# Performance work log

Measured on AMD Instinct MI355X. Metric: run time of the kernel, lower is better.

## Reference

```python
import jax, jax.numpy as jnp
import numpy as np

T, D, H, Z = 16384, 100, 50, 64
LN_EPS = 1e-6


def _ln(x, s, b):
    m = x.mean(-1, keepdims=True)
    v = ((x - m) ** 2).mean(-1, keepdims=True)
    return (x - m) / jnp.sqrt(v + LN_EPS) * s + b


def _gru_ln_scan(y, Wi, Wh, ls, lb):
    # Precompute all input projections once: [T, 3H]
    xi = y @ Wi
    h0 = jnp.zeros((Wh.shape[0],), y.dtype)

    def step(h, xi_t):
        hh = h @ Wh
        xr, xz, xn = jnp.split(xi_t, 3)
        hr, hz, hn = jnp.split(hh, 3)
        r = jax.nn.sigmoid(_ln(xr, ls[0], lb[0]) + _ln(hr, ls[1], lb[1]))
        z = jax.nn.sigmoid(_ln(xz, ls[2], lb[2]) + _ln(hz, ls[3], lb[3]))
        n = jnp.tanh(_ln(xn, ls[4], lb[4]) + r * _ln(hn, ls[5], lb[5]))
        h_new = (1.0 - z) * n + z * h
        return h_new, h_new

    _, hs = jax.lax.scan(step, h0, xi)
    return hs  # [T, H]


def setup_inputs() -> dict:
    key = jax.random.key(0)
    ks = jax.random.split(key, 6)
    sI = 1.0 / jnp.sqrt(jnp.float32(D))
    sH = 1.0 / jnp.sqrt(jnp.float32(H))
    sD = 1.0 / jnp.sqrt(jnp.float32(2 * H))
    return {
        "y": jax.random.normal(ks[0], (T, D), jnp.float32),
        "Wi_f": jax.random.normal(ks[1], (D, 3 * H), jnp.float32) * sI,
        "Wh_f": jax.random.normal(ks[2], (H, 3 * H), jnp.float32) * sH,
        "ln_s_f": jnp.ones((6, H), jnp.float32),
        "ln_b_f": jnp.zeros((6, H), jnp.float32),
        "Wi_b": jax.random.normal(ks[3], (D, 3 * H), jnp.float32) * sI,
        "Wh_b": jax.random.normal(ks[4], (H, 3 * H), jnp.float32) * sH,
        "ln_s_b": jnp.ones((6, H), jnp.float32),
        "ln_b_b": jnp.zeros((6, H), jnp.float32),
        "Wd": jax.random.normal(ks[5], (2 * H, 2 * Z), jnp.float32) * sD,
        "bd": jnp.zeros((2 * Z,), jnp.float32),
    }


def reference(y, Wi_f, Wh_f, ln_s_f, ln_b_f, Wi_b, Wh_b, ln_s_b, ln_b_b, Wd, bd):
    fwd = _gru_ln_scan(y, Wi_f, Wh_f, ln_s_f, ln_b_f)                       # [T, H]
    bwd = jnp.flip(_gru_ln_scan(jnp.flip(y, 0), Wi_b, Wh_b, ln_s_b, ln_b_b), 0)
    cc = jnp.concatenate([fwd, bwd], axis=-1)                               # [T, 2H]
    out = cc @ Wd + bd                                                      # [T, 2Z]
    z = Wd.shape[1] // 2
    mu, vflat = out[:, :z], out[:, z:]
    ev = jnp.exp(vflat)
    eye = jnp.eye(z, dtype=y.dtype)
    Sigma = eye * (ev + 1e-6)[:, None, :]   # diag(exp(v)+1e-6) per timestep
    J = eye * (1.0 / ev)[:, None, :]        # diag(1/exp(v)) per timestep
    h = mu / ev                             # J @ mu for diagonal J
    return Sigma, mu, J, h
```

## Files before the change

### kernel.cpp

```cpp
#include <hip/hip_runtime.h>

#define TT 16384
#define DD 100
#define HH 50
#define XG_STRIDE 160

#define CL 16
#define NCHUNK (TT / CL)
#define BURN 64

#define XROWS 16
#define NFILLB 512

#define WS_XG 0

#define OFF_MU ((size_t)TT * 64 * 64)
#define OFF_J  (OFF_MU + (size_t)TT * 64)
#define OFF_H  (OFF_J + (size_t)TT * 64 * 64)

typedef float v2f __attribute__((ext_vector_type(2)));
typedef float v4f __attribute__((ext_vector_type(4)));

template <int CTRL>
__device__ __forceinline__ float dpp_add(float x) {
    const int y = __builtin_amdgcn_update_dpp(
        0, __builtin_bit_cast(int, x), CTRL, 0xf, 0xf, false);
    return x + __builtin_bit_cast(float, y);
}
__device__ __forceinline__ float wave_sum63(float x) {
    x = dpp_add<0x111>(x);
    x = dpp_add<0x112>(x);
    x = dpp_add<0x114>(x);
    x = dpp_add<0x118>(x);
    x = dpp_add<0x142>(x);
    x = dpp_add<0x143>(x);
    return x;
}
__device__ __forceinline__ float bcast_lane(float x, int l) {
    return __builtin_bit_cast(float,
        __builtin_amdgcn_readlane(__builtin_bit_cast(int, x), l));
}
__device__ __forceinline__ float fold_mean(float w, int L, int lane) {
    const float s = wave_sum63(w);
    const float cm = bcast_lane(s, 63) * 0.02f;
    return (lane == L) ? cm : w;
}

__global__ __launch_bounds__(192) void xprep_kernel(
    const float* __restrict__ y,
    const float* __restrict__ Wi_f, const float* __restrict__ Wi_b,
    const float* __restrict__ ls_f, const float* __restrict__ lb_f,
    const float* __restrict__ ls_b, const float* __restrict__ lb_b,
    float* __restrict__ xg, float* __restrict__ out)
{
    const int tid = threadIdx.x;
    const int dir = blockIdx.y;

    if (dir == 2) {
        const int fb = blockIdx.x;
        v4f* __restrict__ base = (fb < NFILLB)
            ? (v4f*)out : (v4f*)(out + OFF_J);
        const int sub = fb & (NFILLB - 1);
        const long QS = (long)TT * 1024;
        const v4f zz = {0.f, 0.f, 0.f, 0.f};
        const long stride = (long)NFILLB * 192;
        for (long q = (long)sub * 192 + tid; q < QS; q += stride)
            __builtin_nontemporal_store(zz, &base[q]);
        return;
    }

    const int t0  = blockIdx.x * XROWS;
    const float* __restrict__ Wi = dir ? Wi_b : Wi_f;
    const float* __restrict__ ls = dir ? ls_b : ls_f;
    const float* __restrict__ lb = dir ? lb_b : lb_f;

    __shared__ __align__(16) float yst[DD][XROWS];

    for (int idx = tid; idx < DD * XROWS; idx += 192) {
        const int r = idx / DD;
        const int k = idx - r * DD;
        const int row = dir ? (TT - 1 - (t0 + r)) : (t0 + r);
        yst[k][r] = y[(size_t)row * DD + k];
    }
    __syncthreads();

    const int g    = tid >> 6;
    const int lane = tid & 63;
    const bool act = lane < HH;
    const int col  = g * 50 + (act ? lane : 0);

    float acc[XROWS];
    #pragma unroll
    for (int r = 0; r < XROWS; ++r) acc[r] = 0.f;

    #pragma unroll 2
    for (int k = 0; k < DD; ++k) {
        const float w = Wi[k * 150 + col];
        const float4* yr = (const float4*)&yst[k][0];
        const float4 A = yr[0], B = yr[1], C = yr[2], D = yr[3];
        acc[0]  = fmaf(w, A.x, acc[0]);  acc[1]  = fmaf(w, A.y, acc[1]);
        acc[2]  = fmaf(w, A.z, acc[2]);  acc[3]  = fmaf(w, A.w, acc[3]);
        acc[4]  = fmaf(w, B.x, acc[4]);  acc[5]  = fmaf(w, B.y, acc[5]);
        acc[6]  = fmaf(w, B.z, acc[6]);  acc[7]  = fmaf(w, B.w, acc[7]);
        acc[8]  = fmaf(w, C.x, acc[8]);  acc[9]  = fmaf(w, C.y, acc[9]);
        acc[10] = fmaf(w, C.z, acc[10]); acc[11] = fmaf(w, C.w, acc[11]);
        acc[12] = fmaf(w, D.x, acc[12]); acc[13] = fmaf(w, D.y, acc[13]);
        acc[14] = fmaf(w, D.z, acc[14]); acc[15] = fmaf(w, D.w, acc[15]);
    }

    const int lrow = g * 100 + (act ? lane : 0);
    const float sc = ls[lrow], bi = lb[lrow];
    #pragma unroll
    for (int r = 0; r < XROWS; ++r) {
        const float a  = act ? acc[r] : 0.f;
        const float s  = bcast_lane(wave_sum63(a), 63);
        const float s2 = bcast_lane(wave_sum63(a * a), 63);
        const float mean = s * 0.02f;
        const float var  = s2 * 0.02f - mean * mean;
        const float rstd = rsqrtf(var + 1e-6f);
        if (act)
            xg[((size_t)dir * TT + (t0 + r)) * XG_STRIDE + col] =
                (acc[r] - mean) * rstd * sc + bi;
    }
}

__global__ __launch_bounds__(128, 1) void scanhead_kernel(
    const float* __restrict__ xg,
    const float* __restrict__ Wh_f, const float* __restrict__ Wh_b,
    const float* __restrict__ ls_f, const float* __restrict__ lb_f,
    const float* __restrict__ ls_b, const float* __restrict__ lb_b,
    const float* __restrict__ Wd, const float* __restrict__ bd,
    float* __restrict__ out)
{
    const int tid  = threadIdx.x;
    const int wid  = tid >> 6;
    const int lane = tid & 63;
    const int dir  = wid;
    const int blk  = blockIdx.x;

    const float* __restrict__ Wh = dir ? Wh_b : Wh_f;
    const float* __restrict__ ls = dir ? ls_b : ls_f;
    const float* __restrict__ lb = dir ? lb_b : lb_f;
    const float* __restrict__ xgd = xg + (size_t)dir * TT * XG_STRIDE;

    const bool act = lane < HH;

    const int cstart = dir ? (TT - (blk + 1) * CL) : (blk * CL);
    const int rbase  = blk * CL;
    const int t0 = (cstart >= BURN) ? (cstart - BURN) : 0;
    const int tend = cstart + CL;

    __shared__ __align__(16) float ccs[DD][CL];
    __shared__ __align__(16) float os[CL][128];
    __shared__ __align__(16) float hb[2][52];
    if (lane < 52) hb[wid][lane] = 0.f;

    v2f wr2[26], wz2[26], wn2[26];
    #pragma unroll
    for (int p = 0; p < 26; ++p) {
        wr2[p] = (v2f){0.f, 0.f};
        wz2[p] = (v2f){0.f, 0.f};
        wn2[p] = (v2f){0.f, 0.f};
    }
    float s1 = 0.f, b1 = 0.f, s3 = 0.f, b3 = 0.f, s5 = 0.f, b5 = 0.f;
    if (act) {
        #pragma unroll
        for (int k = 0; k < HH; ++k) {
            const float a = Wh[k * 150 + lane];
            const float b = Wh[k * 150 + 50 + lane];
            const float c = Wh[k * 150 + 100 + lane];
            if (k & 1) { wr2[k >> 1].y = a; wz2[k >> 1].y = b; wn2[k >> 1].y = c; }
            else       { wr2[k >> 1].x = a; wz2[k >> 1].x = b; wn2[k >> 1].x = c; }
        }
        s1 = ls[50 + lane];  b1 = lb[50 + lane];
        s3 = ls[150 + lane]; b3 = lb[150 + lane];
        s5 = ls[250 + lane]; b5 = lb[250 + lane];
    }
    #pragma unroll
    for (int p = 0; p < 26; ++p) {
        wr2[p].x = fold_mean(wr2[p].x, 50, lane);
        wr2[p].y = fold_mean(wr2[p].y, 50, lane);
        wz2[p].x = fold_mean(wz2[p].x, 51, lane);
        wz2[p].y = fold_mean(wz2[p].y, 51, lane);
        wn2[p].x = fold_mean(wn2[p].x, 52, lane);
        wn2[p].y = fold_mean(wn2[p].y, 52, lane);
    }

    float hreg = 0.f;
    const int xl = act ? lane : 0;
    const float* __restrict__ x0 = xgd + (size_t)t0 * XG_STRIDE;
    float xr = x0[xl], xz = x0[50 + xl], xn = x0[100 + xl];
    float pxr = x0[XG_STRIDE + xl];
    float pxz = x0[XG_STRIDE + 50 + xl];
    float pxn = x0[XG_STRIDE + 100 + xl];

    #pragma unroll 1
    for (int t = t0; t < tend; ++t) {
        const int tp = (t + 2 < TT) ? (t + 2) : (TT - 1);
        const float* __restrict__ xp = xgd + (size_t)tp * XG_STRIDE;
        const float qxr = xp[xl], qxz = xp[50 + xl], qxn = xp[100 + xl];

        v2f ar0 = {0.f, 0.f}, ar1 = {0.f, 0.f};
        v2f az0 = {0.f, 0.f}, az1 = {0.f, 0.f};
        v2f an0 = {0.f, 0.f}, an1 = {0.f, 0.f};
        const float4* hb4 = reinterpret_cast<const float4*>(&hb[wid][0]);
        #pragma unroll
        for (int q = 0; q < 13; ++q) {
            const float4 hv = hb4[q];
            const v2f h0 = {hv.x, hv.y};
            const v2f h1 = {hv.z, hv.w};
            ar0 = __builtin_elementwise_fma(h0, wr2[2 * q],     ar0);
            ar1 = __builtin_elementwise_fma(h1, wr2[2 * q + 1], ar1);
            az0 = __builtin_elementwise_fma(h0, wz2[2 * q],     az0);
            az1 = __builtin_elementwise_fma(h1, wz2[2 * q + 1], az1);
            an0 = __builtin_elementwise_fma(h0, wn2[2 * q],     an0);
            an1 = __builtin_elementwise_fma(h1, wn2[2 * q + 1], an1);
        }
        const float ar = (ar0.x + ar0.y) + (ar1.x + ar1.y);
        const float az = (az0.x + az0.y) + (az1.x + az1.y);
        const float an = (an0.x + an0.y) + (an1.x + an1.y);

        const float mr = bcast_lane(ar, 50);
        const float mz = bcast_lane(az, 51);
        const float mn = bcast_lane(an, 52);

        const float qrv = act ? ar * ar : 0.f;
        const float qzv = act ? az * az : 0.f;
        const float qnv = act ? an * an : 0.f;
        const float Sr = bcast_lane(wave_sum63(qrv), 63);
        const float Sz = bcast_lane(wave_sum63(qzv), 63);
        const float Sn = bcast_lane(wave_sum63(qnv), 63);

        const float i50 = 0.02f;
        const float vr = fmaf(-mr, mr, Sr * i50);
        const float vz = fmaf(-mz, mz, Sz * i50);
        const float vn = fmaf(-mn, mn, Sn * i50);
        const float rr = rsqrtf(vr + 1e-6f);
        const float rz = rsqrtf(vz + 1e-6f);
        const float rn = rsqrtf(vn + 1e-6f);
        const float hrl = (ar - mr) * rr * s1 + b1;
        const float hzl = (az - mz) * rz * s3 + b3;
        const float hnl = (an - mn) * rn * s5 + b5;

        const float r = __builtin_amdgcn_rcpf(1.f + __expf(-(xr + hrl)));
        const float z = __builtin_amdgcn_rcpf(1.f + __expf(-(xz + hzl)));
        const float e2 = __expf(2.f * (xn + r * hnl));
        const float n = 1.f - 2.f * __builtin_amdgcn_rcpf(e2 + 1.f);
        const float hnew = fmaf(z, hreg - n, n);

        if (act) {
            hb[wid][lane] = hnew;
            if (t >= cstart) {
                const int rr2 = dir ? (TT - 1 - t - rbase) : (t - rbase);
                ccs[dir * 50 + lane][rr2] = hnew;
            }
        }
        hreg = act ? hnew : 0.f;

        xr = pxr; xz = pxz; xn = pxn;
        pxr = qxr; pxz = qxz; pxn = qxn;
    }

    __syncthreads();

    const int j = tid;
    float acc[CL];
    const float bj = bd[j];
    #pragma unroll
    for (int r = 0; r < CL; ++r) acc[r] = bj;

    #pragma unroll 2
    for (int k = 0; k < DD; ++k) {
        const float w = Wd[k * 128 + j];
        const float4* cr = (const float4*)&ccs[k][0];
        const float4 A = cr[0], B4 = cr[1], C4 = cr[2], D4 = cr[3];
        acc[0]  = fmaf(w, A.x,  acc[0]);  acc[1]  = fmaf(w, A.y,  acc[1]);
        acc[2]  = fmaf(w, A.z,  acc[2]);  acc[3]  = fmaf(w, A.w,  acc[3]);
        acc[4]  = fmaf(w, B4.x, acc[4]);  acc[5]  = fmaf(w, B4.y, acc[5]);
        acc[6]  = fmaf(w, B4.z, acc[6]);  acc[7]  = fmaf(w, B4.w, acc[7]);
        acc[8]  = fmaf(w, C4.x, acc[8]);  acc[9]  = fmaf(w, C4.y, acc[9]);
        acc[10] = fmaf(w, C4.z, acc[10]); acc[11] = fmaf(w, C4.w, acc[11]);
        acc[12] = fmaf(w, D4.x, acc[12]); acc[13] = fmaf(w, D4.y, acc[13]);
        acc[14] = fmaf(w, D4.z, acc[14]); acc[15] = fmaf(w, D4.w, acc[15]);
    }
    #pragma unroll
    for (int r = 0; r < CL; ++r) os[r][j] = acc[r];
    __syncthreads();

    if (j < 64) {
        const int d = j & 3;
        #pragma unroll
        for (int r = 0; r < CL; ++r) {
            const int t = rbase + r;
            const float mu  = os[r][j];
            const float evv = __expf(os[r][64 + j]);
            out[OFF_MU + (size_t)t * 64 + j] = mu;
            out[OFF_H  + (size_t)t * 64 + j] = mu / evv;
            const float se = evv + 1e-6f;
            float4 s4;
            s4.x = (d == 0) ? se : 0.f;  s4.y = (d == 1) ? se : 0.f;
            s4.z = (d == 2) ? se : 0.f;  s4.w = (d == 3) ? se : 0.f;
            ((float4*)out)[(size_t)t * 1024 + j * 16 + (j >> 2)] = s4;
        }
    } else {
        const int i = j - 64;
        const int d = i & 3;
        float4* __restrict__ jo4 = (float4*)(out + OFF_J);
        #pragma unroll
        for (int r = 0; r < CL; ++r) {
            const int t = rbase + r;
            const float evv = __expf(os[r][j]);
            const float je = 1.f / evv;
            float4 j4;
            j4.x = (d == 0) ? je : 0.f;  j4.y = (d == 1) ? je : 0.f;
            j4.z = (d == 2) ? je : 0.f;  j4.w = (d == 3) ? je : 0.f;
            jo4[(size_t)t * 1024 + i * 16 + (i >> 2)] = j4;
        }
    }
}

extern "C" void kernel_launch(void* const* d_in, const int* in_sizes, int n_in,
                              void* d_out, int out_size, void* d_ws, size_t ws_size,
                              hipStream_t stream)
{
    const float* y    = (const float*)d_in[0];
    const float* Wi_f = (const float*)d_in[1];
    const float* Wh_f = (const float*)d_in[2];
    const float* ls_f = (const float*)d_in[3];
    const float* lb_f = (const float*)d_in[4];
    const float* Wi_b = (const float*)d_in[5];
    const float* Wh_b = (const float*)d_in[6];
    const float* ls_b = (const float*)d_in[7];
    const float* lb_b = (const float*)d_in[8];
    const float* Wd   = (const float*)d_in[9];
    const float* bd   = (const float*)d_in[10];

    float* out = (float*)d_out;
    float* ws  = (float*)d_ws;
    float* xg  = ws + WS_XG;

    xprep_kernel<<<dim3(TT / XROWS, 3), dim3(192), 0, stream>>>(
        y, Wi_f, Wi_b, ls_f, lb_f, ls_b, lb_b, xg, out);
    scanhead_kernel<<<dim3(NCHUNK), dim3(128), 0, stream>>>(
        xg, Wh_f, Wh_b, ls_f, lb_f, ls_b, lb_b, Wd, bd, out);
}
```

Measured before the change: 248.1 us.

## Use fp16 dot2 recurrent matvec, halve chunk length, raise occupancy

The recurrent weights and the shared hidden-state buffer are stored in fp16, and the per-step matvec uses packed fdot2 with fp32 accumulation instead of fp32 packed FMAs. This halves the register footprint of the weights, which permits launch bounds of 4 blocks per CU. The chunk length drops from 16 to 8, doubling the number of chunks so more scan blocks run in parallel, though the 64-step burn-in is now a larger share of each block's work. The fill-block index is also moved from blockIdx.y 2 to 0. Using fp16 for the hidden state and weights risks precision loss across the recurrence.

```diff
diff --git a/kernel.cpp b/kernel.cpp
--- a/kernel.cpp
+++ b/kernel.cpp
@@ -5,7 +5,7 @@
 #define HH 50
 #define XG_STRIDE 160
 
-#define CL 16
+#define CL 8
 #define NCHUNK (TT / CL)
 #define BURN 64
 
@@ -20,6 +20,7 @@
 
 typedef float v2f __attribute__((ext_vector_type(2)));
 typedef float v4f __attribute__((ext_vector_type(4)));
+typedef _Float16 v2h __attribute__((ext_vector_type(2)));
 
 template <int CTRL>
 __device__ __forceinline__ float dpp_add(float x) {
@@ -54,9 +55,8 @@
     float* __restrict__ xg, float* __restrict__ out)
 {
     const int tid = threadIdx.x;
-    const int dir = blockIdx.y;
-
-    if (dir == 2) {
+
+    if (blockIdx.y == 0) {
         const int fb = blockIdx.x;
         v4f* __restrict__ base = (fb < NFILLB)
             ? (v4f*)out : (v4f*)(out + OFF_J);
@@ -69,6 +69,7 @@
         return;
     }
 
+    const int dir = blockIdx.y - 1;
     const int t0  = blockIdx.x * XROWS;
     const float* __restrict__ Wi = dir ? Wi_b : Wi_f;
     const float* __restrict__ ls = dir ? ls_b : ls_f;
@@ -124,7 +125,7 @@
     }
 }
 
-__global__ __launch_bounds__(128, 1) void scanhead_kernel(
+__global__ __launch_bounds__(128, 4) void scanhead_kernel(
     const float* __restrict__ xg,
     const float* __restrict__ Wh_f, const float* __restrict__ Wh_b,
     const float* __restrict__ ls_f, const float* __restrict__ lb_f,
@@ -152,38 +153,37 @@
 
     __shared__ __align__(16) float ccs[DD][CL];
     __shared__ __align__(16) float os[CL][128];
-    __shared__ __align__(16) float hb[2][52];
-    if (lane < 52) hb[wid][lane] = 0.f;
-
-    v2f wr2[26], wz2[26], wn2[26];
+    __shared__ __align__(16) _Float16 hb[2][64];
+    hb[wid][lane] = (_Float16)0.f;
+
+    v2h wr2[26], wz2[26], wn2[26];
     #pragma unroll
     for (int p = 0; p < 26; ++p) {
-        wr2[p] = (v2f){0.f, 0.f};
-        wz2[p] = (v2f){0.f, 0.f};
-        wn2[p] = (v2f){0.f, 0.f};
-    }
+        const int k0 = 2 * p, k1 = 2 * p + 1;
+        float r0 = 0.f, z0 = 0.f, n0 = 0.f, r1 = 0.f, z1 = 0.f, n1 = 0.f;
+        if (act && k0 < HH) {
+            r0 = Wh[k0 * 150 + lane];
+            z0 = Wh[k0 * 150 + 50 + lane];
+            n0 = Wh[k0 * 150 + 100 + lane];
+        }
+        if (act && k1 < HH) {
+            r1 = Wh[k1 * 150 + lane];
+            z1 = Wh[k1 * 150 + 50 + lane];
+            n1 = Wh[k1 * 150 + 100 + lane];
+        }
+        r0 = fold_mean(r0, 50, lane); r1 = fold_mean(r1, 50, lane);
+        z0 = fold_mean(z0, 51, lane); z1 = fold_mean(z1, 51, lane);
+        n0 = fold_mean(n0, 52, lane); n1 = fold_mean(n1, 52, lane);
+        wr2[p] = (v2h){(_Float16)r0, (_Float16)r1};
+        wz2[p] = (v2h){(_Float16)z0, (_Float16)z1};
+        wn2[p] = (v2h){(_Float16)n0, (_Float16)n1};
+    }
+
     float s1 = 0.f, b1 = 0.f, s3 = 0.f, b3 = 0.f, s5 = 0.f, b5 = 0.f;
     if (act) {
-        #pragma unroll
-        for (int k = 0; k < HH; ++k) {
-            const float a = Wh[k * 150 + lane];
-            const float b = Wh[k * 150 + 50 + lane];
-            const float c = Wh[k * 150 + 100 + lane];
-            if (k & 1) { wr2[k >> 1].y = a; wz2[k >> 1].y = b; wn2[k >> 1].y = c; }
-            else       { wr2[k >> 1].x = a; wz2[k >> 1].x = b; wn2[k >> 1].x = c; }
-        }
         s1 = ls[50 + lane];  b1 = lb[50 + lane];
         s3 = ls[150 + lane]; b3 = lb[150 + lane];
         s5 = ls[250 + lane]; b5 = lb[250 + lane];
-    }
-    #pragma unroll
-    for (int p = 0; p < 26; ++p) {
-        wr2[p].x = fold_mean(wr2[p].x, 50, lane);
-        wr2[p].y = fold_mean(wr2[p].y, 50, lane);
-        wz2[p].x = fold_mean(wz2[p].x, 51, lane);
-        wz2[p].y = fold_mean(wz2[p].y, 51, lane);
-        wn2[p].x = fold_mean(wn2[p].x, 52, lane);
-        wn2[p].y = fold_mean(wn2[p].y, 52, lane);
     }
 
     float hreg = 0.f;
@@ -200,25 +200,31 @@
         const float* __restrict__ xp = xgd + (size_t)tp * XG_STRIDE;
         const float qxr = xp[xl], qxz = xp[50 + xl], qxn = xp[100 + xl];
 
-        v2f ar0 = {0.f, 0.f}, ar1 = {0.f, 0.f};
-        v2f az0 = {0.f, 0.f}, az1 = {0.f, 0.f};
-        v2f an0 = {0.f, 0.f}, an1 = {0.f, 0.f};
-        const float4* hb4 = reinterpret_cast<const float4*>(&hb[wid][0]);
+        const uint4* h4 = (const uint4*)&hb[wid][0];
+        const uint4 a0 = h4[0], a1 = h4[1], a2 = h4[2];
+        const uint4 a3 = h4[3], a4 = h4[4], a5 = h4[5];
+        const uint2 a6 = ((const uint2*)&hb[wid][0])[12];
+        const unsigned hw[26] = {a0.x, a0.y, a0.z, a0.w, a1.x, a1.y, a1.z,
+                                 a1.w, a2.x, a2.y, a2.z, a2.w, a3.x, a3.y,
+                                 a3.z, a3.w, a4.x, a4.y, a4.z, a4.w, a5.x,
+                                 a5.y, a5.z, a5.w, a6.x, a6.y};
+        float c0 = 0.f, c1 = 0.f, d0 = 0.f, d1 = 0.f, e0 = 0.f, e1 = 0.f;
         #pragma unroll
-        for (int q = 0; q < 13; ++q) {
-            const float4 hv = hb4[q];
-            const v2f h0 = {hv.x, hv.y};
-            const v2f h1 = {hv.z, hv.w};
-            ar0 = __builtin_elementwise_fma(h0, wr2[2 * q],     ar0);
-            ar1 = __builtin_elementwise_fma(h1, wr2[2 * q + 1], ar1);
-            az0 = __builtin_elementwise_fma(h0, wz2[2 * q],     az0);
-            az1 = __builtin_elementwise_fma(h1, wz2[2 * q + 1], az1);
-            an0 = __builtin_elementwise_fma(h0, wn2[2 * q],     an0);
-            an1 = __builtin_elementwise_fma(h1, wn2[2 * q + 1], an1);
-        }
-        const float ar = (ar0.x + ar0.y) + (ar1.x + ar1.y);
-        const float az = (az0.x + az0.y) + (az1.x + az1.y);
-        const float an = (an0.x + an0.y) + (an1.x + an1.y);
+        for (int p = 0; p < 26; ++p) {
+            const v2h hp = __builtin_bit_cast(v2h, hw[p]);
+            if (p & 1) {
+                c1 = __builtin_amdgcn_fdot2(hp, wr2[p], c1, false);
+                d1 = __builtin_amdgcn_fdot2(hp, wz2[p], d1, false);
+                e1 = __builtin_amdgcn_fdot2(hp, wn2[p], e1, false);
+            } else {
+                c0 = __builtin_amdgcn_fdot2(hp, wr2[p], c0, false);
+                d0 = __builtin_amdgcn_fdot2(hp, wz2[p], d0, false);
+                e0 = __builtin_amdgcn_fdot2(hp, wn2[p], e0, false);
+            }
+        }
+        const float ar = c0 + c1;
+        const float az = d0 + d1;
+        const float an = e0 + e1;
 
         const float mr = bcast_lane(ar, 50);
         const float mz = bcast_lane(az, 51);
@@ -248,12 +254,11 @@
         const float n = 1.f - 2.f * __builtin_amdgcn_rcpf(e2 + 1.f);
         const float hnew = fmaf(z, hreg - n, n);
 
-        if (act) {
-            hb[wid][lane] = hnew;
-            if (t >= cstart) {
-                const int rr2 = dir ? (TT - 1 - t - rbase) : (t - rbase);
-                ccs[dir * 50 + lane][rr2] = hnew;
-            }
+        const int hidx = act ? lane : 56;
+        hb[wid][hidx] = (_Float16)hnew;
+        if (act && t >= cstart) {
+            const int rr2 = dir ? (TT - 1 - t - rbase) : (t - rbase);
+            ccs[dir * 50 + lane][rr2] = hnew;
         }
         hreg = act ? hnew : 0.f;
 
@@ -273,15 +278,11 @@
     for (int k = 0; k < DD; ++k) {
         const float w = Wd[k * 128 + j];
         const float4* cr = (const float4*)&ccs[k][0];
-        const float4 A = cr[0], B4 = cr[1], C4 = cr[2], D4 = cr[3];
-        acc[0]  = fmaf(w, A.x,  acc[0]);  acc[1]  = fmaf(w, A.y,  acc[1]);
-        acc[2]  = fmaf(w, A.z,  acc[2]);  acc[3]  = fmaf(w, A.w,  acc[3]);
-        acc[4]  = fmaf(w, B4.x, acc[4]);  acc[5]  = fmaf(w, B4.y, acc[5]);
-        acc[6]  = fmaf(w, B4.z, acc[6]);  acc[7]  = fmaf(w, B4.w, acc[7]);
-        acc[8]  = fmaf(w, C4.x, acc[8]);  acc[9]  = fmaf(w, C4.y, acc[9]);
-        acc[10] = fmaf(w, C4.z, acc[10]); acc[11] = fmaf(w, C4.w, acc[11]);
-        acc[12] = fmaf(w, D4.x, acc[12]); acc[13] = fmaf(w, D4.y, acc[13]);
-        acc[14] = fmaf(w, D4.z, acc[14]); acc[15] = fmaf(w, D4.w, acc[15]);
+        const float4 A = cr[0], B4 = cr[1];
+        acc[0] = fmaf(w, A.x,  acc[0]); acc[1] = fmaf(w, A.y,  acc[1]);
+        acc[2] = fmaf(w, A.z,  acc[2]); acc[3] = fmaf(w, A.w,  acc[3]);
+        acc[4] = fmaf(w, B4.x, acc[4]); acc[5] = fmaf(w, B4.y, acc[5]);
+        acc[6] = fmaf(w, B4.z, acc[6]); acc[7] = fmaf(w, B4.w, acc[7]);
     }
     #pragma unroll
     for (int r = 0; r < CL; ++r) os[r][j] = acc[r];
```

Measured after the change: 303.5 us. 22.3% more time.
